# Kernel optimization log

Hardware: AMD Instinct MI355X
Metric: run time of the kernel (lower is better)

The kernel has to match this reference:

```python
import jax, jax.numpy as jnp
import numpy as np

K, NX, NY = 128, 256, 256
MB, NT = 8, 32
D = 3 * K          # ODE state dim (K coefficients per velocity/pressure channel)
H = 128            # MLP hidden width


def setup_inputs() -> dict:
    key = jax.random.key(0)
    ks = jax.random.split(key, 7)
    grid0 = jax.random.normal(ks[0], (MB, 3, NX, NY), dtype=jnp.float32)
    # sorted increasing time grid; small dt keeps random-weight RK4 stable
    t = jnp.arange(NT, dtype=jnp.float32) * 0.01
    init_coeffs = jax.random.normal(ks[1], (D,), dtype=jnp.float32)  # std=1 as in torch init
    W1 = jax.random.normal(ks[2], (H, D), dtype=jnp.float32) * 0.1
    b1 = jnp.zeros((H,), jnp.float32)
    W2 = jax.random.normal(ks[3], (H, H), dtype=jnp.float32) * 0.1
    b2 = jnp.zeros((H,), jnp.float32)
    W3 = jax.random.normal(ks[4], (D, H), dtype=jnp.float32) * 0.1
    b3 = jnp.zeros((D,), jnp.float32)
    basis = jax.random.normal(ks[5], (K, 3, NX, NY), dtype=jnp.float32)  # stacked basis_fns
    return dict(grid0=grid0, t=t, init_coeffs=init_coeffs,
                W1=W1, b1=b1, W2=W2, b2=b2, W3=W3, b3=b3, basis=basis)


def reference(grid0, t, init_coeffs, W1, b1, W2, b2, W3, b3, basis):
    mb = grid0.shape[0]
    nt = t.shape[0]

    def mlp(c):  # ODEFunc.net: Linear-ReLU-Linear-ELU-Linear (t is ignored)
        h = jax.nn.relu(c @ W1.T + b1)
        h = jax.nn.elu(h @ W2.T + b2)
        return h @ W3.T + b3

    y0 = jnp.tile(init_coeffs[None, :], (mb, 1))  # (mb, 3K)

    # torchdiffeq fixed-grid 'rk4' = 3/8-rule step between consecutive t points
    def step(y, ts):
        t0, t1 = ts
        dt = t1 - t0
        k1 = mlp(y)
        k2 = mlp(y + dt * k1 / 3.0)
        k3 = mlp(y + dt * (k2 - k1 / 3.0))
        k4 = mlp(y + dt * (k1 - k2 + k3))
        y1 = y + dt * (k1 + 3.0 * (k2 + k3) + k4) * 0.125
        return y1, y1

    _, ys = jax.lax.scan(step, y0, (t[:-1], t[1:]))
    coeff = jnp.concatenate([y0[None], ys], axis=0)          # (nt, mb, 3K)
    coeff = coeff.reshape(nt, mb, K, 3)

    # soln = sum_k w_k(t) * f_k(x,y), fused contraction over K experts
    soln = jnp.einsum('tmkc,kcxy->tmcxy', coeff, basis)       # (nt, mb, 3, nx, ny)
    return soln
```

## Files before the change

kernel.cpp:

```cpp
#include <hip/hip_runtime.h>
#include <hip/hip_bf16.h>
#include <math.h>

#define NT 32
#define NSTEP 31
#define DD 384
#define HH 128
#define KK 128
#define MBATCH 8
#define NPIX 65536
#define NUNITS 768
#define EBLOCKS 255
#define FLAG_OFF 49152

typedef float f32x4 __attribute__((ext_vector_type(4)));
typedef short bf16x8 __attribute__((ext_vector_type(8)));

__device__ __forceinline__ unsigned cvtpk(float a, float b) {
  unsigned r;
  asm("v_cvt_pk_bf16_f32 %0, %1, %2" : "=v"(r) : "v"(a), "v"(b));
  return r;
}
__device__ __forceinline__ unsigned short f2bf(float f) {
  return (unsigned short)(cvtpk(f, 0.f) & 0xFFFFu);
}

__global__ __launch_bounds__(512, 1) void fused_kernel(
    const float* __restrict__ tarr, const float* __restrict__ ic,
    const float* __restrict__ W1, const float* __restrict__ b1,
    const float* __restrict__ W2, const float* __restrict__ b2,
    const float* __restrict__ W3, const float* __restrict__ b3,
    const float* __restrict__ basis,
    float* __restrict__ coeffT, int* __restrict__ flagp,
    float* __restrict__ out)
{
  __shared__ bf16x8 sh_w1[8 * 12 * 64];
  __shared__ __align__(16) float sh_y[DD];
  __shared__ __align__(16) float sh_k[4][DD];
  __shared__ __align__(16) float sh_b1[HH], sh_b2[HH], sh_b3[DD];
  __shared__ float sh_t[NT];
  __shared__ __align__(16) unsigned short sh_x[DD];
  __shared__ __align__(16) unsigned sh_h1u[HH / 2];
  __shared__ __align__(16) unsigned sh_h2u[HH / 2];

  const int tid = threadIdx.x;

  if (blockIdx.x == 0) {
    const int w = tid >> 6, l = tid & 63;
    const int r16 = l & 15, g = l >> 4;

    for (int i = tid; i < HH; i += 512) { sh_b1[i] = b1[i]; sh_b2[i] = b2[i]; }
    for (int i = tid; i < DD; i += 512) {
      sh_b3[i] = b3[i];
      float y0 = ic[i];
      sh_y[i] = y0;
      sh_x[i] = f2bf(y0);
      coeffT[(i % 3) * (KK * NT) + (i / 3) * NT + 0] = y0;
    }
    if (tid < NT) sh_t[tid] = tarr[tid];

    for (int idx = tid; idx < 8 * 12 * 64; idx += 512) {
      const int lw = idx & 63, tmp = idx >> 6;
      const int c = tmp % 12, ww = tmp / 12;
      const float* src = W1 + (16 * ww + (lw & 15)) * DD + 32 * c + 8 * (lw >> 4);
      bf16x8 v;
      #pragma unroll
      for (int j = 0; j < 8; ++j) v[j] = (short)f2bf(src[j]);
      sh_w1[idx] = v;
    }

    bf16x8 w2f[4], w3f[3][4];
    #pragma unroll
    for (int c = 0; c < 4; ++c) {
      const float* src = W2 + (16 * w + r16) * HH + 32 * c + 8 * g;
      #pragma unroll
      for (int j = 0; j < 8; ++j) w2f[c][j] = (short)f2bf(src[j]);
    }
    #pragma unroll
    for (int t3 = 0; t3 < 3; ++t3)
      #pragma unroll
      for (int c = 0; c < 4; ++c) {
        const float* src = W3 + (48 * w + 16 * t3 + r16) * HH + 32 * c + 8 * g;
        #pragma unroll
        for (int j = 0; j < 8; ++j) w3f[t3][c][j] = (short)f2bf(src[j]);
      }

    __syncthreads();

    for (int step = 0; step < NSTEP; ++step) {
      const float dt  = sh_t[step + 1] - sh_t[step];
      const float dt3 = dt * (1.0f / 3.0f);
      #pragma unroll
      for (int s = 0; s < 4; ++s) {
        if (s > 0) {
          if (tid < DD) {
            float y = sh_y[tid], x;
            if (s == 1)      x = fmaf(dt3, sh_k[0][tid], y);
            else if (s == 2) x = fmaf(dt, sh_k[1][tid] - (1.0f/3.0f) * sh_k[0][tid], y);
            else             x = fmaf(dt, sh_k[0][tid] - sh_k[1][tid] + sh_k[2][tid], y);
            sh_x[tid] = f2bf(x);
          }
          __syncthreads();
        }

        {
          f32x4 a0 = {0.f,0.f,0.f,0.f}, a1 = {0.f,0.f,0.f,0.f};
          f32x4 a2 = {0.f,0.f,0.f,0.f}, a3 = {0.f,0.f,0.f,0.f};
          #pragma unroll
          for (int c = 0; c < 12; c += 4) {
            bf16x8 A0 = sh_w1[(w * 12 + c + 0) * 64 + l];
            bf16x8 B0 = *(const bf16x8*)&sh_x[(c + 0) * 32 + g * 8];
            a0 = __builtin_amdgcn_mfma_f32_16x16x32_bf16(A0, B0, a0, 0, 0, 0);
            bf16x8 A1 = sh_w1[(w * 12 + c + 1) * 64 + l];
            bf16x8 B1 = *(const bf16x8*)&sh_x[(c + 1) * 32 + g * 8];
            a1 = __builtin_amdgcn_mfma_f32_16x16x32_bf16(A1, B1, a1, 0, 0, 0);
            bf16x8 A2 = sh_w1[(w * 12 + c + 2) * 64 + l];
            bf16x8 B2 = *(const bf16x8*)&sh_x[(c + 2) * 32 + g * 8];
            a2 = __builtin_amdgcn_mfma_f32_16x16x32_bf16(A2, B2, a2, 0, 0, 0);
            bf16x8 A3 = sh_w1[(w * 12 + c + 3) * 64 + l];
            bf16x8 B3 = *(const bf16x8*)&sh_x[(c + 3) * 32 + g * 8];
            a3 = __builtin_amdgcn_mfma_f32_16x16x32_bf16(A3, B3, a3, 0, 0, 0);
          }
          if (r16 == 0) {
            f32x4 bv = *(const f32x4*)&sh_b1[16 * w + 4 * g];
            float h0 = fmaxf(a0[0] + a1[0] + a2[0] + a3[0] + bv[0], 0.f);
            float h1_ = fmaxf(a0[1] + a1[1] + a2[1] + a3[1] + bv[1], 0.f);
            float h2_ = fmaxf(a0[2] + a1[2] + a2[2] + a3[2] + bv[2], 0.f);
            float h3 = fmaxf(a0[3] + a1[3] + a2[3] + a3[3] + bv[3], 0.f);
            const int base = (16 * w + 4 * g) >> 1;
            sh_h1u[base]     = cvtpk(h0, h1_);
            sh_h1u[base + 1] = cvtpk(h2_, h3);
          }
        }
        __syncthreads();

        {
          f32x4 acc0 = {0.f,0.f,0.f,0.f}, acc1 = {0.f,0.f,0.f,0.f};
          acc0 = __builtin_amdgcn_mfma_f32_16x16x32_bf16(
              w2f[0], *(const bf16x8*)&sh_h1u[0 * 16 + g * 4], acc0, 0, 0, 0);
          acc1 = __builtin_amdgcn_mfma_f32_16x16x32_bf16(
              w2f[1], *(const bf16x8*)&sh_h1u[1 * 16 + g * 4], acc1, 0, 0, 0);
          acc0 = __builtin_amdgcn_mfma_f32_16x16x32_bf16(
              w2f[2], *(const bf16x8*)&sh_h1u[2 * 16 + g * 4], acc0, 0, 0, 0);
          acc1 = __builtin_amdgcn_mfma_f32_16x16x32_bf16(
              w2f[3], *(const bf16x8*)&sh_h1u[3 * 16 + g * 4], acc1, 0, 0, 0);
          if (r16 == 0) {
            f32x4 bv = *(const f32x4*)&sh_b2[16 * w + 4 * g];
            float v0 = acc0[0] + acc1[0] + bv[0];
            float v1 = acc0[1] + acc1[1] + bv[1];
            float v2 = acc0[2] + acc1[2] + bv[2];
            float v3 = acc0[3] + acc1[3] + bv[3];
            v0 = v0 > 0.f ? v0 : (__expf(v0) - 1.0f);
            v1 = v1 > 0.f ? v1 : (__expf(v1) - 1.0f);
            v2 = v2 > 0.f ? v2 : (__expf(v2) - 1.0f);
            v3 = v3 > 0.f ? v3 : (__expf(v3) - 1.0f);
            const int base = (16 * w + 4 * g) >> 1;
            sh_h2u[base]     = cvtpk(v0, v1);
            sh_h2u[base + 1] = cvtpk(v2, v3);
          }
        }
        __syncthreads();

        {
          bf16x8 bb0 = *(const bf16x8*)&sh_h2u[0 * 16 + g * 4];
          bf16x8 bb1 = *(const bf16x8*)&sh_h2u[1 * 16 + g * 4];
          bf16x8 bb2 = *(const bf16x8*)&sh_h2u[2 * 16 + g * 4];
          bf16x8 bb3 = *(const bf16x8*)&sh_h2u[3 * 16 + g * 4];
          f32x4 ka[3];
          #pragma unroll
          for (int t3 = 0; t3 < 3; ++t3) {
            f32x4 acc = {0.f, 0.f, 0.f, 0.f};
            acc = __builtin_amdgcn_mfma_f32_16x16x32_bf16(w3f[t3][0], bb0, acc, 0, 0, 0);
            acc = __builtin_amdgcn_mfma_f32_16x16x32_bf16(w3f[t3][1], bb1, acc, 0, 0, 0);
            acc = __builtin_amdgcn_mfma_f32_16x16x32_bf16(w3f[t3][2], bb2, acc, 0, 0, 0);
            acc = __builtin_amdgcn_mfma_f32_16x16x32_bf16(w3f[t3][3], bb3, acc, 0, 0, 0);
            ka[t3] = acc;
          }
          if (r16 == 0) {
            #pragma unroll
            for (int t3 = 0; t3 < 3; ++t3) {
              const int row0 = 48 * w + 16 * t3 + 4 * g;
              f32x4 bv = *(const f32x4*)&sh_b3[row0];
              f32x4 kv;
              kv[0] = ka[t3][0] + bv[0]; kv[1] = ka[t3][1] + bv[1];
              kv[2] = ka[t3][2] + bv[2]; kv[3] = ka[t3][3] + bv[3];
              *(f32x4*)&sh_k[s][row0] = kv;
            }
          }
        }
        __syncthreads();
      }

      if (tid < DD) {
        float y = sh_y[tid];
        y = fmaf(dt * 0.125f,
                 sh_k[0][tid] + 3.f * (sh_k[1][tid] + sh_k[2][tid]) + sh_k[3][tid], y);
        sh_y[tid] = y;
        sh_x[tid] = f2bf(y);
        coeffT[(tid % 3) * (KK * NT) + (tid / 3) * NT + (step + 1)] = y;
      }
      __syncthreads();

      if (((step + 2) & 3) == 0 && tid == 0) {
        __threadfence();
        __hip_atomic_store(flagp, step + 2, __ATOMIC_RELEASE,
                           __HIP_MEMORY_SCOPE_AGENT);
      }
    }

    __threadfence();
    if (tid == 0)
      __hip_atomic_store(flagp, NT, __ATOMIC_RELEASE, __HIP_MEMORY_SCOPE_AGENT);

  } else {
    const int Wv   = tid >> 6;
    const int lane = tid & 63;
    const int half = lane >> 5;
    const int slot = lane & 31;
    const int t_a  = 4 * Wv + 2 * half;
    const int need = 4 * Wv + 4;

    int polls = 0;
    while (__hip_atomic_load(flagp, __ATOMIC_RELAXED,
                             __HIP_MEMORY_SCOPE_AGENT) < need) {
      __builtin_amdgcn_s_sleep(127);
      if ((++polls & 31) == 0)
        (void)__hip_atomic_load(flagp, __ATOMIC_ACQUIRE,
                                __HIP_MEMORY_SCOPE_AGENT);
    }
    while (__hip_atomic_load(flagp, __ATOMIC_ACQUIRE,
                             __HIP_MEMORY_SCOPE_AGENT) < need)
      __builtin_amdgcn_s_sleep(8);

    for (int u = (int)blockIdx.x - 1; u < NUNITS; u += EBLOCKS) {
      const int c = u >> 8, ptile = u & 255;
      const int px0 = ptile * 256 + slot * 8;
      const float* bp = basis + (size_t)c * NPIX + px0;
      const float* cT = coeffT + c * (KK * NT) + t_a;

      float acc[2][8];
      #pragma unroll
      for (int h = 0; h < 2; ++h)
        #pragma unroll
        for (int p = 0; p < 8; ++p) acc[h][p] = 0.f;

      #pragma unroll 4
      for (int k = 0; k < KK; ++k) {
        const float* bk = bp + (size_t)k * (3 * NPIX);
        float4 b0 = *(const float4*)(bk);
        float4 b1v = *(const float4*)(bk + 4);
        float2 cv = *(const float2*)(cT + k * NT);
        float bs[8] = {b0.x, b0.y, b0.z, b0.w, b1v.x, b1v.y, b1v.z, b1v.w};
        #pragma unroll
        for (int p = 0; p < 8; ++p) {
          acc[0][p] = fmaf(cv.x, bs[p], acc[0][p]);
          acc[1][p] = fmaf(cv.y, bs[p], acc[1][p]);
        }
      }

      #pragma unroll
      for (int h = 0; h < 2; ++h) {
        const int tt = t_a + h;
        float4 lo = make_float4(acc[h][0], acc[h][1], acc[h][2], acc[h][3]);
        float4 hi = make_float4(acc[h][4], acc[h][5], acc[h][6], acc[h][7]);
        #pragma unroll
        for (int m = 0; m < MBATCH; ++m) {
          float* op = out + (((size_t)(tt * MBATCH + m) * 3 + c) << 16) + px0;
          *(float4*)(op)     = lo;
          *(float4*)(op + 4) = hi;
        }
      }
    }
  }
}

extern "C" void kernel_launch(void* const* d_in, const int* in_sizes, int n_in,
                              void* d_out, int out_size, void* d_ws, size_t ws_size,
                              hipStream_t stream) {
  (void)in_sizes; (void)n_in; (void)out_size; (void)ws_size;
  const float* tarr  = (const float*)d_in[1];
  const float* ic    = (const float*)d_in[2];
  const float* W1    = (const float*)d_in[3];
  const float* b1    = (const float*)d_in[4];
  const float* W2    = (const float*)d_in[5];
  const float* b2    = (const float*)d_in[6];
  const float* W3    = (const float*)d_in[7];
  const float* b3    = (const float*)d_in[8];
  const float* basis = (const float*)d_in[9];
  float* coeffT = (float*)d_ws;
  int*   flagp  = (int*)((char*)d_ws + FLAG_OFF);
  float* out    = (float*)d_out;

  (void)hipMemsetAsync((void*)flagp, 0, 64, stream);

  hipLaunchKernelGGL(fused_kernel, dim3(256), dim3(512), 0, stream,
                     tarr, ic, W1, b1, W2, b2, W3, b3, basis,
                     coeffT, flagp, out);
}
```

Baseline: 253.1 us.

## Keep most W1 fragments in registers and restructure expansion into time-phased passes

The ODE block now holds 8 of the 12 W1 column chunks in registers and keeps only the last 4 in shared memory, which cuts LDS traffic in the first MLP layer. The expansion blocks change from waiting for their wave's timesteps and then handling 2 timesteps by 8 pixels per thread. Each block now runs four phases, each waiting for a group of 8 timesteps and handling 1 timestep by 4 pixels per thread. Expansion work can start after the first 8 steps instead of blocking per wave, but the basis is re-read once per phase (4x basis traffic) and register pressure in block 0 rises.

```diff
diff --git a/kernel.cpp b/kernel.cpp
--- a/kernel.cpp
+++ b/kernel.cpp
@@ -34,7 +34,7 @@
     float* __restrict__ coeffT, int* __restrict__ flagp,
     float* __restrict__ out)
 {
-  __shared__ bf16x8 sh_w1[8 * 12 * 64];
+  __shared__ bf16x8 sh_w1[8 * 4 * 64];
   __shared__ __align__(16) float sh_y[DD];
   __shared__ __align__(16) float sh_k[4][DD];
   __shared__ __align__(16) float sh_b1[HH], sh_b2[HH], sh_b3[DD];
@@ -59,17 +59,23 @@
     }
     if (tid < NT) sh_t[tid] = tarr[tid];
 
-    for (int idx = tid; idx < 8 * 12 * 64; idx += 512) {
+    for (int idx = tid; idx < 8 * 4 * 64; idx += 512) {
       const int lw = idx & 63, tmp = idx >> 6;
-      const int c = tmp % 12, ww = tmp / 12;
-      const float* src = W1 + (16 * ww + (lw & 15)) * DD + 32 * c + 8 * (lw >> 4);
+      const int cc = tmp % 4, ww = tmp / 4;
+      const float* src = W1 + (16 * ww + (lw & 15)) * DD + 32 * (8 + cc) + 8 * (lw >> 4);
       bf16x8 v;
       #pragma unroll
       for (int j = 0; j < 8; ++j) v[j] = (short)f2bf(src[j]);
       sh_w1[idx] = v;
     }
 
-    bf16x8 w2f[4], w3f[3][4];
+    bf16x8 w1f[8], w2f[4], w3f[3][4];
+    #pragma unroll
+    for (int c = 0; c < 8; ++c) {
+      const float* src = W1 + (16 * w + r16) * DD + 32 * c + 8 * g;
+      #pragma unroll
+      for (int j = 0; j < 8; ++j) w1f[c][j] = (short)f2bf(src[j]);
+    }
     #pragma unroll
     for (int c = 0; c < 4; ++c) {
       const float* src = W2 + (16 * w + r16) * HH + 32 * c + 8 * g;
@@ -107,18 +113,28 @@
           f32x4 a0 = {0.f,0.f,0.f,0.f}, a1 = {0.f,0.f,0.f,0.f};
           f32x4 a2 = {0.f,0.f,0.f,0.f}, a3 = {0.f,0.f,0.f,0.f};
           #pragma unroll
-          for (int c = 0; c < 12; c += 4) {
-            bf16x8 A0 = sh_w1[(w * 12 + c + 0) * 64 + l];
+          for (int c = 0; c < 8; c += 4) {
             bf16x8 B0 = *(const bf16x8*)&sh_x[(c + 0) * 32 + g * 8];
+            a0 = __builtin_amdgcn_mfma_f32_16x16x32_bf16(w1f[c + 0], B0, a0, 0, 0, 0);
+            bf16x8 B1 = *(const bf16x8*)&sh_x[(c + 1) * 32 + g * 8];
+            a1 = __builtin_amdgcn_mfma_f32_16x16x32_bf16(w1f[c + 1], B1, a1, 0, 0, 0);
+            bf16x8 B2 = *(const bf16x8*)&sh_x[(c + 2) * 32 + g * 8];
+            a2 = __builtin_amdgcn_mfma_f32_16x16x32_bf16(w1f[c + 2], B2, a2, 0, 0, 0);
+            bf16x8 B3 = *(const bf16x8*)&sh_x[(c + 3) * 32 + g * 8];
+            a3 = __builtin_amdgcn_mfma_f32_16x16x32_bf16(w1f[c + 3], B3, a3, 0, 0, 0);
+          }
+          {
+            bf16x8 A0 = sh_w1[(w * 4 + 0) * 64 + l];
+            bf16x8 B0 = *(const bf16x8*)&sh_x[8 * 32 + g * 8];
             a0 = __builtin_amdgcn_mfma_f32_16x16x32_bf16(A0, B0, a0, 0, 0, 0);
-            bf16x8 A1 = sh_w1[(w * 12 + c + 1) * 64 + l];
-            bf16x8 B1 = *(const bf16x8*)&sh_x[(c + 1) * 32 + g * 8];
+            bf16x8 A1 = sh_w1[(w * 4 + 1) * 64 + l];
+            bf16x8 B1 = *(const bf16x8*)&sh_x[9 * 32 + g * 8];
             a1 = __builtin_amdgcn_mfma_f32_16x16x32_bf16(A1, B1, a1, 0, 0, 0);
-            bf16x8 A2 = sh_w1[(w * 12 + c + 2) * 64 + l];
-            bf16x8 B2 = *(const bf16x8*)&sh_x[(c + 2) * 32 + g * 8];
+            bf16x8 A2 = sh_w1[(w * 4 + 2) * 64 + l];
+            bf16x8 B2 = *(const bf16x8*)&sh_x[10 * 32 + g * 8];
             a2 = __builtin_amdgcn_mfma_f32_16x16x32_bf16(A2, B2, a2, 0, 0, 0);
-            bf16x8 A3 = sh_w1[(w * 12 + c + 3) * 64 + l];
-            bf16x8 B3 = *(const bf16x8*)&sh_x[(c + 3) * 32 + g * 8];
+            bf16x8 A3 = sh_w1[(w * 4 + 3) * 64 + l];
+            bf16x8 B3 = *(const bf16x8*)&sh_x[11 * 32 + g * 8];
             a3 = __builtin_amdgcn_mfma_f32_16x16x32_bf16(A3, B3, a3, 0, 0, 0);
           }
           if (r16 == 0) {
@@ -215,59 +231,43 @@
   } else {
     const int Wv   = tid >> 6;
     const int lane = tid & 63;
-    const int half = lane >> 5;
-    const int slot = lane & 31;
-    const int t_a  = 4 * Wv + 2 * half;
-    const int need = 4 * Wv + 4;
-
-    int polls = 0;
-    while (__hip_atomic_load(flagp, __ATOMIC_RELAXED,
-                             __HIP_MEMORY_SCOPE_AGENT) < need) {
-      __builtin_amdgcn_s_sleep(127);
-      if ((++polls & 31) == 0)
-        (void)__hip_atomic_load(flagp, __ATOMIC_ACQUIRE,
-                                __HIP_MEMORY_SCOPE_AGENT);
-    }
-    while (__hip_atomic_load(flagp, __ATOMIC_ACQUIRE,
-                             __HIP_MEMORY_SCOPE_AGENT) < need)
-      __builtin_amdgcn_s_sleep(8);
-
-    for (int u = (int)blockIdx.x - 1; u < NUNITS; u += EBLOCKS) {
-      const int c = u >> 8, ptile = u & 255;
-      const int px0 = ptile * 256 + slot * 8;
-      const float* bp = basis + (size_t)c * NPIX + px0;
-      const float* cT = coeffT + c * (KK * NT) + t_a;
-
-      float acc[2][8];
-      #pragma unroll
-      for (int h = 0; h < 2; ++h)
-        #pragma unroll
-        for (int p = 0; p < 8; ++p) acc[h][p] = 0.f;
-
-      #pragma unroll 4
-      for (int k = 0; k < KK; ++k) {
-        const float* bk = bp + (size_t)k * (3 * NPIX);
-        float4 b0 = *(const float4*)(bk);
-        float4 b1v = *(const float4*)(bk + 4);
-        float2 cv = *(const float2*)(cT + k * NT);
-        float bs[8] = {b0.x, b0.y, b0.z, b0.w, b1v.x, b1v.y, b1v.z, b1v.w};
-        #pragma unroll
-        for (int p = 0; p < 8; ++p) {
-          acc[0][p] = fmaf(cv.x, bs[p], acc[0][p]);
-          acc[1][p] = fmaf(cv.y, bs[p], acc[1][p]);
-        }
-      }
-
-      #pragma unroll
-      for (int h = 0; h < 2; ++h) {
-        const int tt = t_a + h;
-        float4 lo = make_float4(acc[h][0], acc[h][1], acc[h][2], acc[h][3]);
-        float4 hi = make_float4(acc[h][4], acc[h][5], acc[h][6], acc[h][7]);
+    const int slot = Wv * 8 + (lane & 7);
+    const int tq   = lane >> 3;
+
+    for (int o = 0; o < 4; ++o) {
+      const int need = 8 * (o + 1);
+      int polls = 0;
+      while (__hip_atomic_load(flagp, __ATOMIC_RELAXED,
+                               __HIP_MEMORY_SCOPE_AGENT) < need) {
+        __builtin_amdgcn_s_sleep(127);
+        if ((++polls & 31) == 0)
+          (void)__hip_atomic_load(flagp, __ATOMIC_ACQUIRE,
+                                  __HIP_MEMORY_SCOPE_AGENT);
+      }
+      while (__hip_atomic_load(flagp, __ATOMIC_ACQUIRE,
+                               __HIP_MEMORY_SCOPE_AGENT) < need)
+        __builtin_amdgcn_s_sleep(8);
+
+      const int t = 8 * o + tq;
+      for (int u = (int)blockIdx.x - 1; u < NUNITS; u += EBLOCKS) {
+        const int c = u >> 8, ptile = u & 255;
+        const int px0 = ptile * 256 + slot * 4;
+        const float* bp = basis + (size_t)c * NPIX + px0;
+        const float* cT = coeffT + c * (KK * NT) + t;
+
+        float a0 = 0.f, a1 = 0.f, a2 = 0.f, a3 = 0.f;
+        #pragma unroll 4
+        for (int k = 0; k < KK; ++k) {
+          float4 b = *(const float4*)(bp + (size_t)k * (3 * NPIX));
+          float cv = cT[k * NT];
+          a0 = fmaf(cv, b.x, a0); a1 = fmaf(cv, b.y, a1);
+          a2 = fmaf(cv, b.z, a2); a3 = fmaf(cv, b.w, a3);
+        }
+        float4 r = make_float4(a0, a1, a2, a3);
         #pragma unroll
         for (int m = 0; m < MBATCH; ++m) {
-          float* op = out + (((size_t)(tt * MBATCH + m) * 3 + c) << 16) + px0;
-          *(float4*)(op)     = lo;
-          *(float4*)(op + 4) = hi;
+          float* op = out + (((size_t)((t * MBATCH + m) * 3 + c)) << 16) + px0;
+          *(float4*)op = r;
         }
       }
     }
```

Result: slower. 290.8 us (+14.9%).

## Spread final-timestep expansion across all waves instead of one tail wave

Applied to the files above, without the earlier changes.

Previously wave 7 of each expansion block alone handled timesteps 28-31. It could only start once the ODE integration had fully finished, so that work sat serially at the end of the kernel. Now waves 0-6 still expand their own timestep groups as the coefficients become ready. After the final flag, all eight waves split the last four timesteps by pixel halves using narrower float2 loads. This is meant to shorten the post-ODE tail on the critical path, at the cost of less vectorised loads and more coefficient reads in that final phase.

```diff
diff --git a/kernel.cpp b/kernel.cpp
--- a/kernel.cpp
+++ b/kernel.cpp
@@ -23,6 +23,20 @@
 }
 __device__ __forceinline__ unsigned short f2bf(float f) {
   return (unsigned short)(cvtpk(f, 0.f) & 0xFFFFu);
+}
+
+__device__ __forceinline__ void wait_flag(int* flagp, int need) {
+  int polls = 0;
+  while (__hip_atomic_load(flagp, __ATOMIC_RELAXED,
+                           __HIP_MEMORY_SCOPE_AGENT) < need) {
+    __builtin_amdgcn_s_sleep(127);
+    if ((++polls & 31) == 0)
+      (void)__hip_atomic_load(flagp, __ATOMIC_ACQUIRE,
+                              __HIP_MEMORY_SCOPE_AGENT);
+  }
+  while (__hip_atomic_load(flagp, __ATOMIC_ACQUIRE,
+                           __HIP_MEMORY_SCOPE_AGENT) < need)
+    __builtin_amdgcn_s_sleep(8);
 }
 
 __global__ __launch_bounds__(512, 1) void fused_kernel(
@@ -215,59 +229,78 @@
   } else {
     const int Wv   = tid >> 6;
     const int lane = tid & 63;
-    const int half = lane >> 5;
-    const int slot = lane & 31;
-    const int t_a  = 4 * Wv + 2 * half;
-    const int need = 4 * Wv + 4;
-
-    int polls = 0;
-    while (__hip_atomic_load(flagp, __ATOMIC_RELAXED,
-                             __HIP_MEMORY_SCOPE_AGENT) < need) {
-      __builtin_amdgcn_s_sleep(127);
-      if ((++polls & 31) == 0)
-        (void)__hip_atomic_load(flagp, __ATOMIC_ACQUIRE,
-                                __HIP_MEMORY_SCOPE_AGENT);
-    }
-    while (__hip_atomic_load(flagp, __ATOMIC_ACQUIRE,
-                             __HIP_MEMORY_SCOPE_AGENT) < need)
-      __builtin_amdgcn_s_sleep(8);
-
-    for (int u = (int)blockIdx.x - 1; u < NUNITS; u += EBLOCKS) {
-      const int c = u >> 8, ptile = u & 255;
-      const int px0 = ptile * 256 + slot * 8;
-      const float* bp = basis + (size_t)c * NPIX + px0;
-      const float* cT = coeffT + c * (KK * NT) + t_a;
-
-      float acc[2][8];
-      #pragma unroll
-      for (int h = 0; h < 2; ++h)
+
+    if (Wv < 7) {
+      const int half = lane >> 5;
+      const int slot = lane & 31;
+      const int t_a  = 4 * Wv + 2 * half;
+      wait_flag(flagp, 4 * Wv + 4);
+
+      for (int u = (int)blockIdx.x - 1; u < NUNITS; u += EBLOCKS) {
+        const int c = u >> 8, ptile = u & 255;
+        const int px0 = ptile * 256 + slot * 8;
+        const float* bp = basis + (size_t)c * NPIX + px0;
+        const float* cT = coeffT + c * (KK * NT) + t_a;
+
+        float acc[2][8];
         #pragma unroll
-        for (int p = 0; p < 8; ++p) acc[h][p] = 0.f;
-
-      #pragma unroll 4
-      for (int k = 0; k < KK; ++k) {
-        const float* bk = bp + (size_t)k * (3 * NPIX);
-        float4 b0 = *(const float4*)(bk);
-        float4 b1v = *(const float4*)(bk + 4);
-        float2 cv = *(const float2*)(cT + k * NT);
-        float bs[8] = {b0.x, b0.y, b0.z, b0.w, b1v.x, b1v.y, b1v.z, b1v.w};
+        for (int h = 0; h < 2; ++h)
+          #pragma unroll
+          for (int p = 0; p < 8; ++p) acc[h][p] = 0.f;
+
+        #pragma unroll 4
+        for (int k = 0; k < KK; ++k) {
+          const float* bk = bp + (size_t)k * (3 * NPIX);
+          float4 b0 = *(const float4*)(bk);
+          float4 b1v = *(const float4*)(bk + 4);
+          float2 cv = *(const float2*)(cT + k * NT);
+          float bs[8] = {b0.x, b0.y, b0.z, b0.w, b1v.x, b1v.y, b1v.z, b1v.w};
+          #pragma unroll
+          for (int p = 0; p < 8; ++p) {
+            acc[0][p] = fmaf(cv.x, bs[p], acc[0][p]);
+            acc[1][p] = fmaf(cv.y, bs[p], acc[1][p]);
+          }
+        }
+
         #pragma unroll
-        for (int p = 0; p < 8; ++p) {
-          acc[0][p] = fmaf(cv.x, bs[p], acc[0][p]);
-          acc[1][p] = fmaf(cv.y, bs[p], acc[1][p]);
-        }
-      }
-
-      #pragma unroll
-      for (int h = 0; h < 2; ++h) {
-        const int tt = t_a + h;
-        float4 lo = make_float4(acc[h][0], acc[h][1], acc[h][2], acc[h][3]);
-        float4 hi = make_float4(acc[h][4], acc[h][5], acc[h][6], acc[h][7]);
+        for (int h = 0; h < 2; ++h) {
+          const int tt = t_a + h;
+          float4 lo = make_float4(acc[h][0], acc[h][1], acc[h][2], acc[h][3]);
+          float4 hi = make_float4(acc[h][4], acc[h][5], acc[h][6], acc[h][7]);
+          #pragma unroll
+          for (int m = 0; m < MBATCH; ++m) {
+            float* op = out + (((size_t)(tt * MBATCH + m) * 3 + c) << 16) + px0;
+            *(float4*)(op)     = lo;
+            *(float4*)(op + 4) = hi;
+          }
+        }
+      }
+    }
+
+    {
+      const int t   = 28 + (Wv & 3);
+      const int phx = (Wv >> 2) * 128;
+      wait_flag(flagp, NT);
+
+      for (int u = (int)blockIdx.x - 1; u < NUNITS; u += EBLOCKS) {
+        const int c = u >> 8, ptile = u & 255;
+        const int px0 = ptile * 256 + phx + lane * 2;
+        const float* bp = basis + (size_t)c * NPIX + px0;
+        const float* cT = coeffT + c * (KK * NT) + t;
+
+        float a0 = 0.f, a1 = 0.f;
+        #pragma unroll 8
+        for (int k = 0; k < KK; ++k) {
+          float2 b = *(const float2*)(bp + (size_t)k * (3 * NPIX));
+          float cv = cT[k * NT];
+          a0 = fmaf(cv, b.x, a0);
+          a1 = fmaf(cv, b.y, a1);
+        }
+        float2 r = make_float2(a0, a1);
         #pragma unroll
         for (int m = 0; m < MBATCH; ++m) {
-          float* op = out + (((size_t)(tt * MBATCH + m) * 3 + c) << 16) + px0;
-          *(float4*)(op)     = lo;
-          *(float4*)(op + 4) = hi;
+          float* op = out + (((size_t)((t * MBATCH + m) * 3 + c)) << 16) + px0;
+          *(float2*)op = r;
         }
       }
     }
```

New measurement: 269.7 us. 1.07x slower.
